# Kernel tuning notes

Hardware: AMD Instinct MI355X
Metric: run time of the kernel (lower is better)

Reference implementation:

```python
import jax, jax.numpy as jnp
import numpy as np

B, C, H, W = 2, 128, 64, 256
G, P, EXP = 8, 4, 2
D = C // G


def _conv1x1(x, w, b):
    # x: (b,c,h,w), w: (o,c), b: (o,)
    return jnp.einsum('bchw,oc->bohw', x, w) + b[None, :, None, None]


def _lin_sample(value, x):
    # value: (b,g,d,h,w); x: (b,g,p,h,w) pixel coords along W -> (b,g,d,p,h,w)
    Bv, Gv, Dv, Hv, Wv = value.shape
    Pv = x.shape[2]
    xc = jnp.clip(x, 0.0, Wv - 1.0)
    x0 = jnp.floor(xc)
    i0 = x0.astype(jnp.int32)
    i1 = jnp.minimum(i0 + 1, Wv - 1)
    t = (xc - x0)[:, :, None]  # (b,g,1,p,h,w)
    shape = (Bv, Gv, Dv, Pv, Hv, Wv)
    v = jnp.broadcast_to(value[:, :, :, None], shape)
    v0 = jnp.take_along_axis(v, jnp.broadcast_to(i0[:, :, None], shape), axis=-1)
    v1 = jnp.take_along_axis(v, jnp.broadcast_to(i1[:, :, None], shape), axis=-1)
    return v0 * (1.0 - t) + v1 * t


def _layernorm_c(x, g, b):
    mu = jnp.mean(x, axis=1, keepdims=True)
    var = jnp.mean((x - mu) ** 2, axis=1, keepdims=True)
    return (x - mu) * jax.lax.rsqrt(var + 1e-5) * g[None, :, None, None] + b[None, :, None, None]


def _forward(ml, mr, fl, fr, nl, nr, gml, gmr, cap, gap,
             wv, bv, wn, bn, woc, boc, wog, bog, wa, ba, wo, bo,
             lw, lb, w1, b1, w2, b2):
    mask = jnp.concatenate([gml, gmr], axis=0)   # (2B,1,H,W)
    q = jnp.concatenate([ml, mr], axis=0)        # (2B,C,H,W)
    ctx = jnp.concatenate([fr, fl], axis=0)      # cross: right feats for left queries
    geo = jnp.concatenate([nr, nl], axis=0)      # (2B,3,H,W)
    B2 = q.shape[0]
    # deformable 1D cross-attention (normal-guided)
    value = _conv1x1(ctx, wv, bv).reshape(B2, G, D, H, W)
    nfeat = _conv1x1(geo, wn, bn).reshape(B2, G, D, H, W)
    off_c = _conv1x1(q, woc, boc).reshape(B2, G, P, H, W)
    off_g = _conv1x1(q, wog, bog).reshape(B2, G, P, H, W)
    attn = jax.nn.softmax(_conv1x1(q, wa, ba).reshape(B2, G, 2 * P, H, W), axis=2)
    ctx_kp = jnp.clip(cap * (W - 1.0) + off_c, 0.0, W - 1.0)
    geo_kp = jnp.clip(gap * (W - 1.0) + off_g, 0.0, W - 1.0)
    s_ctx = _lin_sample(value, ctx_kp)           # (2B,G,D,P,H,W)
    s_geo = _lin_sample(nfeat, geo_kp)
    sampled = jnp.concatenate([s_ctx, s_geo], axis=3)  # (2B,G,D,2P,H,W)
    agg = jnp.einsum('bgdphw,bgphw->bgdhw', sampled, attn).reshape(B2, C, H, W)
    upd = _conv1x1(agg, wo, bo) * mask
    # residual + LayerNorm over channels + 1x1-conv FFN
    x = q + upd
    x = _layernorm_c(x, lw, lb)
    h1 = _conv1x1(x, w1, b1)
    x = x + _conv1x1(h1 * jax.nn.sigmoid(h1), w2, b2)
    return x, ctx_kp, geo_kp


def setup_inputs() -> dict:
    key = jax.random.key(0)
    ks = jax.random.split(key, 20)
    f32 = jnp.float32
    def n(k, shape, s=1.0):
        return jax.random.normal(k, shape, dtype=f32) * s
    return {
        'match_left': n(ks[0], (B, C, H, W)),
        'match_right': n(ks[1], (B, C, H, W)),
        'feat_left': n(ks[2], (B, C, H, W)),
        'feat_right': n(ks[3], (B, C, H, W)),
        'normal_left': n(ks[4], (B, 3, H, W)),
        'normal_right': n(ks[5], (B, 3, H, W)),
        'gate_mask_left': jax.random.uniform(ks[6], (B, 1, H, W), dtype=f32),
        'gate_mask_right': jax.random.uniform(ks[7], (B, 1, H, W), dtype=f32),
        'context_anchor_points': jax.random.uniform(ks[8], (2 * B, G, P, H, W), dtype=f32),
        'geometric_anchor_points': jax.random.uniform(ks[9], (2 * B, G, P, H, W), dtype=f32),
        'w_value': n(ks[10], (C, C), 0.02), 'b_value': jnp.zeros((C,), f32),
        'w_normal': n(ks[11], (C, 3), 0.02), 'b_normal': jnp.zeros((C,), f32),
        'w_off_ctx': n(ks[12], (G * P, C), 0.02), 'b_off_ctx': jnp.zeros((G * P,), f32),
        'w_off_geo': n(ks[13], (G * P, C), 0.02), 'b_off_geo': jnp.zeros((G * P,), f32),
        'w_attn': n(ks[14], (G * 2 * P, C), 0.02), 'b_attn': jnp.zeros((G * 2 * P,), f32),
        'w_out': n(ks[15], (C, C), 0.02), 'b_out': jnp.zeros((C,), f32),
        'ln_w': jnp.ones((C,), f32), 'ln_b': jnp.zeros((C,), f32),
        'w_ff1': n(ks[16], (EXP * C, C), 0.02), 'b_ff1': jnp.zeros((EXP * C,), f32),
        'w_ff2': n(ks[17], (C, EXP * C), 0.02), 'b_ff2': jnp.zeros((C,), f32),
    }


def reference(match_left, match_right, feat_left, feat_right, normal_left, normal_right,
              gate_mask_left, gate_mask_right, context_anchor_points, geometric_anchor_points,
              w_value, b_value, w_normal, b_normal, w_off_ctx, b_off_ctx, w_off_geo, b_off_geo,
              w_attn, b_attn, w_out, b_out, ln_w, ln_b, w_ff1, b_ff1, w_ff2, b_ff2):
    x, ckp, gkp = _forward(match_left, match_right, feat_left, feat_right, normal_left, normal_right,
                           gate_mask_left, gate_mask_right, context_anchor_points, geometric_anchor_points,
                           w_value, b_value, w_normal, b_normal, w_off_ctx, b_off_ctx, w_off_geo, b_off_geo,
                           w_attn, b_attn, w_out, b_out, ln_w, ln_b, w_ff1, b_ff1, w_ff2, b_ff2)
    ml, mr = jnp.split(x, 2, axis=0)
    return (ml, mr, ckp, gkp)
```

## Files before the change

### kernel.cpp

```cpp
#include <hip/hip_runtime.h>
#include <cstdint>
#include <math.h>

#define B2v 4
#define Cc  128
#define Hh  64
#define Ww  256
#define Gg  8
#define Pp  4
#define HW  (Hh*Ww)
#define CHW (Cc*HW)
#define PIT 136

typedef float f32x4 __attribute__((ext_vector_type(4)));
typedef short s16x8 __attribute__((ext_vector_type(8)));
typedef short s16x4 __attribute__((ext_vector_type(4)));

__device__ __forceinline__ short f2bf(float x) {
    union { float f; unsigned u; } a; a.f = x;
    unsigned r = a.u + 0x7fffu + ((a.u >> 16) & 1u);
    return (short)(r >> 16);
}
__device__ __forceinline__ float bf2f(short s) {
    union { unsigned u; float f; } a; a.u = ((unsigned)(unsigned short)s) << 16;
    return a.f;
}
__device__ __forceinline__ unsigned pack2_bf(float f0, float f1) {
    union { float f; unsigned u; } a, b; a.f = f0; b.f = f1;
    return __builtin_amdgcn_perm(b.u, a.u, 0x07060302);
}

__global__ __launch_bounds__(256) void prep_kernel(
    const float* __restrict__ wv, const float* __restrict__ woc,
    const float* __restrict__ wog, const float* __restrict__ wa,
    const float* __restrict__ wo, const float* __restrict__ w1,
    const float* __restrict__ w2,
    const float* __restrict__ boc, const float* __restrict__ bog,
    const float* __restrict__ ba,
    short* __restrict__ wbf, float* __restrict__ bq)
{
    int i = blockIdx.x * 256 + threadIdx.x;
    if (i < 16384) wbf[i] = f2bf(wv[i]);
    else if (i < 32768) {
        int j = i - 16384; int r = j >> 7, c = j & 127;
        float v = (r < 32) ? woc[r * 128 + c] : (r < 64) ? wog[(r - 32) * 128 + c]
                                              : wa[(r - 64) * 128 + c];
        wbf[i] = f2bf(v);
    }
    else if (i < 49152)  wbf[i] = f2bf(wo[i - 32768]);
    else if (i < 81920)  wbf[i] = f2bf(w1[i - 49152]);
    else if (i < 114688) wbf[i] = f2bf(w2[i - 81920]);
    else if (i < 114816) {
        int r = i - 114688;
        bq[r] = (r < 32) ? boc[r] : (r < 64) ? bog[r - 32] : ba[r - 64];
    }
}

__global__ __launch_bounds__(512, 2) void mega_kernel(
    const float* __restrict__ mlq, const float* __restrict__ mrq,
    const float* __restrict__ fl,  const float* __restrict__ fr,
    const float* __restrict__ nl,  const float* __restrict__ nr,
    const float* __restrict__ gml, const float* __restrict__ gmr,
    const float* __restrict__ cap, const float* __restrict__ gap,
    const short* __restrict__ wbf, const float* __restrict__ bq,
    const float* __restrict__ bv,
    const float* __restrict__ wn,  const float* __restrict__ bn,
    const float* __restrict__ bo,
    const float* __restrict__ lnw, const float* __restrict__ lnb,
    const float* __restrict__ b1,  const float* __restrict__ b2,
    float* __restrict__ out_ml, float* __restrict__ out_mr,
    float* __restrict__ ckp_out, float* __restrict__ gkp_out)
{
    __shared__ short buf1[256 * PIT];
    __shared__ short buf2[256 * PIT];
    __shared__ float sgeo[3 * 256];
    __shared__ float swn4[128 * 4];
    __shared__ float redS[512], redQ[512];
    __shared__ float smu[256], srs[256];

    const short* wv_bf = wbf;
    const short* wq_bf = wbf + 16384;
    const short* wo_bf = wbf + 32768;
    const short* w1_bf = wbf + 49152;
    const short* w2_bf = wbf + 81920;

    const int t    = threadIdx.x;
    const int lane = t & 63;
    const int ww   = t >> 6;
    const int lm   = lane & 15;
    const int lq   = lane >> 4;
    const int h = blockIdx.x, b = blockIdx.y;
    const int hWw = h * Ww;
    const int px   = t & 255;
    const int half = t >> 8;

    const float* ctx = (b < 2) ? fr + (size_t)b * CHW : fl + (size_t)(b - 2) * CHW;
    const float* q   = (b < 2) ? mlq + (size_t)b * CHW : mrq + (size_t)(b - 2) * CHW;
    const float* geo = (b < 2) ? nr + (size_t)b * 3 * HW : nl + (size_t)(b - 2) * 3 * HW;
    const float* msk = (b < 2) ? gml + (size_t)b * HW : gmr + (size_t)(b - 2) * HW;
    float* outp = (b < 2) ? out_ml + (size_t)b * CHW : out_mr + (size_t)(b - 2) * CHW;

    for (int i = t; i < 768; i += 512) sgeo[i] = geo[(size_t)(i >> 8) * HW + hWw + (i & 255)];
    if (t < 128) {
        swn4[t * 4 + 0] = wn[t * 3 + 0];
        swn4[t * 4 + 1] = wn[t * 3 + 1];
        swn4[t * 4 + 2] = wn[t * 3 + 2];
        swn4[t * 4 + 3] = bn[t];
    }

    {
        const int c0 = ww * 16;
#pragma unroll
        for (int sub = 0; sub < 4; sub++) {
            const int p = sub * 64 + lane;
            const size_t base = (size_t)c0 * HW + hWw + p;
#pragma unroll
            for (int k = 0; k < 8; k++) {
                float f0 = ctx[base + (size_t)(2 * k) * HW];
                float f1 = ctx[base + (size_t)(2 * k + 1) * HW];
                *(unsigned*)(&buf1[p * PIT + c0 + 2 * k]) = pack2_bf(f0, f1);
            }
        }
    }
    __syncthreads();

    {
        f32x4 acc[16];
#pragma unroll
        for (int nt = 0; nt < 16; nt++) acc[nt] = (f32x4){0.f, 0.f, 0.f, 0.f};
#pragma unroll
        for (int kk = 0; kk < 4; kk++) {
            s16x8 a = *(const s16x8*)(wv_bf + (size_t)(ww * 16 + lm) * 128 + kk * 32 + lq * 8);
#pragma unroll
            for (int nt = 0; nt < 16; nt++) {
                s16x8 bfv = *(const s16x8*)(&buf1[(nt * 16 + lm) * PIT + kk * 32 + lq * 8]);
                acc[nt] = __builtin_amdgcn_mfma_f32_16x16x32_bf16(a, bfv, acc[nt], 0, 0, 0);
            }
        }
        const int ob = ww * 16 + lq * 4;
        float bias[4];
#pragma unroll
        for (int r = 0; r < 4; r++) bias[r] = bv[ob + r];
#pragma unroll
        for (int nt = 0; nt < 16; nt++) {
            const int wg = nt * 16 + lm;
            s16x4 pk;
#pragma unroll
            for (int r = 0; r < 4; r++) pk[r] = f2bf(acc[nt][r] + bias[r]);
            *(s16x4*)(&buf2[wg * PIT + ob]) = pk;
        }
    }
    __syncthreads();

    {
        const int c0 = ww * 16;
#pragma unroll
        for (int sub = 0; sub < 4; sub++) {
            const int p = sub * 64 + lane;
            const size_t base = (size_t)c0 * HW + hWw + p;
#pragma unroll
            for (int k = 0; k < 8; k++) {
                float f0 = q[base + (size_t)(2 * k) * HW];
                float f1 = q[base + (size_t)(2 * k + 1) * HW];
                *(unsigned*)(&buf1[p * PIT + c0 + 2 * k]) = pack2_bf(f0, f1);
            }
        }
    }
    __syncthreads();

    {
        f32x4 acc[16];
#pragma unroll
        for (int nt = 0; nt < 16; nt++) acc[nt] = (f32x4){0.f, 0.f, 0.f, 0.f};
#pragma unroll
        for (int kk = 0; kk < 4; kk++) {
            s16x8 a = *(const s16x8*)(wq_bf + (size_t)(ww * 16 + lm) * 128 + kk * 32 + lq * 8);
#pragma unroll
            for (int nt = 0; nt < 16; nt++) {
                s16x8 bfv = *(const s16x8*)(&buf1[(nt * 16 + lm) * PIT + kk * 32 + lq * 8]);
                acc[nt] = __builtin_amdgcn_mfma_f32_16x16x32_bf16(a, bfv, acc[nt], 0, 0, 0);
            }
        }
        __syncthreads();
        const int ob = ww * 16 + lq * 4;
        float bias[4];
#pragma unroll
        for (int r = 0; r < 4; r++) bias[r] = bq[ob + r];
#pragma unroll
        for (int nt = 0; nt < 16; nt++) {
            const int wg = nt * 16 + lm;
            s16x4 pk;
#pragma unroll
            for (int r = 0; r < 4; r++) pk[r] = f2bf(acc[nt][r] + bias[r]);
            *(s16x4*)(&buf1[wg * PIT + ob]) = pk;
        }
    }
    __syncthreads();

    float attnr[4][8], kpr[4][8];
#pragma unroll
    for (int gi = 0; gi < 4; gi++) {
        const int g = half * 4 + gi;
        s16x8 lg = *(const s16x8*)(&buf1[px * PIT + 64 + g * 8]);
        float L[8], m = -1e30f;
#pragma unroll
        for (int j = 0; j < 8; j++) { L[j] = bf2f(lg[j]); m = fmaxf(m, L[j]); }
        float s = 0.f;
#pragma unroll
        for (int j = 0; j < 8; j++) { L[j] = expf(L[j] - m); s += L[j]; }
        float inv = 1.f / s;
#pragma unroll
        for (int j = 0; j < 8; j++) attnr[gi][j] = L[j] * inv;
#pragma unroll
        for (int p = 0; p < 4; p++) {
            size_t kidx = ((((size_t)b * Gg + g) * Pp + p) * Hh + h) * Ww + px;
            float oc = bf2f(buf1[px * PIT + g * 4 + p]);
            float og = bf2f(buf1[px * PIT + 32 + g * 4 + p]);
            float ck = fminf(fmaxf(cap[kidx] * 255.0f + oc, 0.f), 255.f);
            float gk = fminf(fmaxf(gap[kidx] * 255.0f + og, 0.f), 255.f);
            ckp_out[kidx] = ck;
            gkp_out[kidx] = gk;
            kpr[gi][p] = ck;
            kpr[gi][4 + p] = gk;
        }
    }
    __syncthreads();

#pragma unroll
    for (int gi = 0; gi < 4; gi++) {
        const int g = half * 4 + gi;
        float a16[16];
#pragma unroll
        for (int d = 0; d < 16; d++) a16[d] = 0.f;
#pragma unroll
        for (int j = 0; j < 4; j++) {
            float x = kpr[gi][j];
            int i0 = (int)floorf(x);
            int i1 = min(i0 + 1, Ww - 1);
            float tt = x - (float)i0;
            float c0 = attnr[gi][j] * (1.f - tt);
            float c1 = attnr[gi][j] * tt;
            s16x8 v0a = *(const s16x8*)(&buf2[i0 * PIT + g * 16]);
            s16x8 v0b = *(const s16x8*)(&buf2[i0 * PIT + g * 16 + 8]);
            s16x8 v1a = *(const s16x8*)(&buf2[i1 * PIT + g * 16]);
            s16x8 v1b = *(const s16x8*)(&buf2[i1 * PIT + g * 16 + 8]);
#pragma unroll
            for (int d = 0; d < 8; d++) {
                a16[d]     += c0 * bf2f(v0a[d]) + c1 * bf2f(v1a[d]);
                a16[8 + d] += c0 * bf2f(v0b[d]) + c1 * bf2f(v1b[d]);
            }
        }
        {
            float gs0 = 0.f, gs1 = 0.f, gs2 = 0.f, as = 0.f;
#pragma unroll
            for (int j = 4; j < 8; j++) {
                float x = kpr[gi][j];
                int i0 = (int)floorf(x);
                int i1 = min(i0 + 1, Ww - 1);
                float tt = x - (float)i0;
                float c0 = attnr[gi][j] * (1.f - tt);
                float c1 = attnr[gi][j] * tt;
                gs0 += c0 * sgeo[i0] + c1 * sgeo[i1];
                gs1 += c0 * sgeo[256 + i0] + c1 * sgeo[256 + i1];
                gs2 += c0 * sgeo[512 + i0] + c1 * sgeo[512 + i1];
                as  += attnr[gi][j];
            }
#pragma unroll
            for (int d = 0; d < 16; d++) {
                const float* w4 = &swn4[(g * 16 + d) * 4];
                a16[d] += w4[0] * gs0 + w4[1] * gs1 + w4[2] * gs2 + w4[3] * as;
            }
        }
        s16x8 p0, p1;
#pragma unroll
        for (int d = 0; d < 8; d++) { p0[d] = f2bf(a16[d]); p1[d] = f2bf(a16[8 + d]); }
        *(s16x8*)(&buf1[px * PIT + g * 16])     = p0;
        *(s16x8*)(&buf1[px * PIT + g * 16 + 8]) = p1;
    }
    __syncthreads();

    {
        f32x4 acc1[16];
#pragma unroll
        for (int nt = 0; nt < 16; nt++) acc1[nt] = (f32x4){0.f, 0.f, 0.f, 0.f};
#pragma unroll
        for (int kk = 0; kk < 4; kk++) {
            s16x8 a = *(const s16x8*)(wo_bf + (size_t)(ww * 16 + lm) * 128 + kk * 32 + lq * 8);
#pragma unroll
            for (int nt = 0; nt < 16; nt++) {
                s16x8 bfv = *(const s16x8*)(&buf1[(nt * 16 + lm) * PIT + kk * 32 + lq * 8]);
                acc1[nt] = __builtin_amdgcn_mfma_f32_16x16x32_bf16(a, bfv, acc1[nt], 0, 0, 0);
            }
        }
        __syncthreads();
        const int ob = ww * 16 + lq * 4;
        float bias[4];
#pragma unroll
        for (int r = 0; r < 4; r++) bias[r] = bo[ob + r];
#pragma unroll
        for (int nt = 0; nt < 16; nt++) {
            const int wg = nt * 16 + lm;
            float mval = msk[hWw + wg];
            s16x4 pk;
#pragma unroll
            for (int r = 0; r < 4; r++) {
                float upd = acc1[nt][r] + bias[r];
                float qv = q[(size_t)(ob + r) * HW + hWw + wg];
                pk[r] = f2bf(qv + upd * mval);
            }
            *(s16x4*)(&buf1[wg * PIT + ob]) = pk;
        }
    }
    __syncthreads();

    {
        float ls = 0.f, lsq = 0.f;
#pragma unroll
        for (int c8 = 0; c8 < 8; c8++) {
            s16x8 v = *(const s16x8*)(&buf1[px * PIT + half * 64 + c8 * 8]);
#pragma unroll
            for (int j = 0; j < 8; j++) { float f = bf2f(v[j]); ls += f; lsq += f * f; }
        }
        redS[t] = ls; redQ[t] = lsq;
        __syncthreads();
        if (t < 256) {
            float s  = redS[t] + redS[t + 256];
            float qq = redQ[t] + redQ[t + 256];
            float mu = s * (1.f / 128.f);
            float var = qq * (1.f / 128.f) - mu * mu;
            smu[t] = mu;
            srs[t] = rsqrtf(var + 1e-5f);
        }
        __syncthreads();
        const float mu = smu[px], rs = srs[px];
#pragma unroll
        for (int c8 = 0; c8 < 8; c8++) {
            s16x8 v = *(const s16x8*)(&buf1[px * PIT + half * 64 + c8 * 8]);
            s16x8 pk;
#pragma unroll
            for (int j = 0; j < 8; j++) {
                int c = half * 64 + c8 * 8 + j;
                pk[j] = f2bf((bf2f(v[j]) - mu) * rs * lnw[c] + lnb[c]);
            }
            *(s16x8*)(&buf1[px * PIT + half * 64 + c8 * 8]) = pk;
        }
    }
    __syncthreads();

    f32x4 acc3[16];
#pragma unroll
    for (int nt = 0; nt < 16; nt++) acc3[nt] = (f32x4){0.f, 0.f, 0.f, 0.f};

    for (int jc = 0; jc < 2; jc++) {
        f32x4 acc2[16];
#pragma unroll
        for (int nt = 0; nt < 16; nt++) acc2[nt] = (f32x4){0.f, 0.f, 0.f, 0.f};
#pragma unroll
        for (int kk = 0; kk < 4; kk++) {
            s16x8 a = *(const s16x8*)(w1_bf + (size_t)(jc * 128 + ww * 16 + lm) * 128 + kk * 32 + lq * 8);
#pragma unroll
            for (int nt = 0; nt < 16; nt++) {
                s16x8 bfv = *(const s16x8*)(&buf1[(nt * 16 + lm) * PIT + kk * 32 + lq * 8]);
                acc2[nt] = __builtin_amdgcn_mfma_f32_16x16x32_bf16(a, bfv, acc2[nt], 0, 0, 0);
            }
        }
        {
            const int jb = ww * 16 + lq * 4;
            float bias[4];
#pragma unroll
            for (int r = 0; r < 4; r++) bias[r] = b1[jc * 128 + jb + r];
#pragma unroll
            for (int nt = 0; nt < 16; nt++) {
                const int wg = nt * 16 + lm;
                s16x4 pk;
#pragma unroll
                for (int r = 0; r < 4; r++) {
                    float hv = acc2[nt][r] + bias[r];
                    pk[r] = f2bf(hv / (1.f + expf(-hv)));
                }
                *(s16x4*)(&buf2[wg * PIT + jb]) = pk;
            }
        }
        __syncthreads();
#pragma unroll
        for (int kk = 0; kk < 4; kk++) {
            s16x8 a = *(const s16x8*)(w2_bf + (size_t)(ww * 16 + lm) * 256 + jc * 128 + kk * 32 + lq * 8);
#pragma unroll
            for (int nt = 0; nt < 16; nt++) {
                s16x8 bfv = *(const s16x8*)(&buf2[(nt * 16 + lm) * PIT + kk * 32 + lq * 8]);
                acc3[nt] = __builtin_amdgcn_mfma_f32_16x16x32_bf16(a, bfv, acc3[nt], 0, 0, 0);
            }
        }
        __syncthreads();
    }

    {
        const int ob = ww * 16 + lq * 4;
        float b2v[4];
#pragma unroll
        for (int r = 0; r < 4; r++) b2v[r] = b2[ob + r];
#pragma unroll
        for (int nt = 0; nt < 16; nt++) {
            const int wg = nt * 16 + lm;
            s16x4 xn4 = *(const s16x4*)(&buf1[wg * PIT + ob]);
#pragma unroll
            for (int r = 0; r < 4; r++)
                outp[(size_t)(ob + r) * HW + hWw + wg] = bf2f(xn4[r]) + b2v[r] + acc3[nt][r];
        }
    }
}

extern "C" void kernel_launch(void* const* d_in, const int* in_sizes, int n_in,
                              void* d_out, int out_size, void* d_ws, size_t ws_size,
                              hipStream_t stream)
{
    const float* match_l = (const float*)d_in[0];
    const float* match_r = (const float*)d_in[1];
    const float* feat_l  = (const float*)d_in[2];
    const float* feat_r  = (const float*)d_in[3];
    const float* norm_l  = (const float*)d_in[4];
    const float* norm_r  = (const float*)d_in[5];
    const float* gml     = (const float*)d_in[6];
    const float* gmr     = (const float*)d_in[7];
    const float* cap     = (const float*)d_in[8];
    const float* gap     = (const float*)d_in[9];
    const float* wv  = (const float*)d_in[10]; const float* bv  = (const float*)d_in[11];
    const float* wn  = (const float*)d_in[12]; const float* bn  = (const float*)d_in[13];
    const float* woc = (const float*)d_in[14]; const float* boc = (const float*)d_in[15];
    const float* wog = (const float*)d_in[16]; const float* bog = (const float*)d_in[17];
    const float* wa  = (const float*)d_in[18]; const float* ba  = (const float*)d_in[19];
    const float* wo  = (const float*)d_in[20]; const float* bo  = (const float*)d_in[21];
    const float* lnw = (const float*)d_in[22]; const float* lnb = (const float*)d_in[23];
    const float* w1  = (const float*)d_in[24]; const float* b1  = (const float*)d_in[25];
    const float* w2  = (const float*)d_in[26]; const float* b2  = (const float*)d_in[27];

    float* out = (float*)d_out;
    float* out_ml  = out;
    float* out_mr  = out + (size_t)2 * CHW;
    float* ckp_out = out + (size_t)4 * CHW;
    float* gkp_out = ckp_out + (size_t)B2v * Gg * Pp * HW;

    float* ws = (float*)d_ws;
    float* bq  = ws;
    short* wbf = (short*)(bq + 128);

    prep_kernel<<<dim3(449), dim3(256), 0, stream>>>(
        wv, woc, wog, wa, wo, w1, w2, boc, bog, ba, wbf, bq);
    mega_kernel<<<dim3(Hh, B2v), dim3(512), 0, stream>>>(
        match_l, match_r, feat_l, feat_r, norm_l, norm_r, gml, gmr, cap, gap,
        wbf, bq, bv, wn, bn, bo, lnw, lnb, b1, b2,
        out_ml, out_mr, ckp_out, gkp_out);
}
```

Baseline: 223.6 us.

## Vectorize input staging, merge GEMM phases, use hardware bf16 pack and fast math

Loads ctx and q with float4 global reads into two separate LDS buffers in a single phase, which drops two barriers and lets the value and query projections run back to back. It prefetches anchor points into registers, packs LDS constants (geo as float4, normal weights as pairs, LN params), and converts to bf16 with the v_cvt_pk_bf16_f32 instruction. It also swaps expf, division and rsqrt for the fast hardware intrinsics, and uses packed float2 math in the sampling loop. The costs are higher register pressure from the prefetched arrays and slightly lower precision in softmax, SiLU and LayerNorm.

```diff
diff --git a/kernel.cpp b/kernel.cpp
--- a/kernel.cpp
+++ b/kernel.cpp
@@ -13,6 +13,7 @@
 #define PIT 136
 
 typedef float f32x4 __attribute__((ext_vector_type(4)));
+typedef float f32x2 __attribute__((ext_vector_type(2)));
 typedef short s16x8 __attribute__((ext_vector_type(8)));
 typedef short s16x4 __attribute__((ext_vector_type(4)));
 
@@ -25,10 +26,18 @@
     union { unsigned u; float f; } a; a.u = ((unsigned)(unsigned short)s) << 16;
     return a.f;
 }
-__device__ __forceinline__ unsigned pack2_bf(float f0, float f1) {
-    union { float f; unsigned u; } a, b; a.f = f0; b.f = f1;
-    return __builtin_amdgcn_perm(b.u, a.u, 0x07060302);
-}
+__device__ __forceinline__ unsigned cvtpk(float lo, float hi) {
+    unsigned r;
+    asm("v_cvt_pk_bf16_f32 %0, %1, %2" : "=v"(r) : "v"(lo), "v"(hi));
+    return r;
+}
+__device__ __forceinline__ f32x2 unpk(unsigned w) {
+    union { unsigned u; float f; } lo, hi;
+    lo.u = w << 16; hi.u = w & 0xffff0000u;
+    return (f32x2){lo.f, hi.f};
+}
+__device__ __forceinline__ float frcp(float x) { return __builtin_amdgcn_rcpf(x); }
+__device__ __forceinline__ float fexp(float x) { return __expf(x); }
 
 __global__ __launch_bounds__(256) void prep_kernel(
     const float* __restrict__ wv, const float* __restrict__ woc,
@@ -73,8 +82,9 @@
 {
     __shared__ short buf1[256 * PIT];
     __shared__ short buf2[256 * PIT];
-    __shared__ float sgeo[3 * 256];
-    __shared__ float swn4[128 * 4];
+    __shared__ f32x4 sgeo4[256];
+    __shared__ f32x2 swnp[256];
+    __shared__ float sln[256];
     __shared__ float redS[512], redQ[512];
     __shared__ float smu[256], srs[256];
 
@@ -100,43 +110,81 @@
     const float* msk = (b < 2) ? gml + (size_t)b * HW : gmr + (size_t)(b - 2) * HW;
     float* outp = (b < 2) ? out_ml + (size_t)b * CHW : out_mr + (size_t)(b - 2) * CHW;
 
-    for (int i = t; i < 768; i += 512) sgeo[i] = geo[(size_t)(i >> 8) * HW + hWw + (i & 255)];
-    if (t < 128) {
-        swn4[t * 4 + 0] = wn[t * 3 + 0];
-        swn4[t * 4 + 1] = wn[t * 3 + 1];
-        swn4[t * 4 + 2] = wn[t * 3 + 2];
-        swn4[t * 4 + 3] = bn[t];
+    float capr[16], gapr[16];
+    const size_t kbase = ((size_t)b * Gg + half * 4) * Pp * (size_t)HW + hWw + px;
+    {
+#pragma unroll
+        for (int i = 0; i < 16; i++) {
+            capr[i] = cap[kbase + (size_t)i * HW];
+            gapr[i] = gap[kbase + (size_t)i * HW];
+        }
+    }
+
+    if (t < 256) {
+        sgeo4[t] = (f32x4){geo[hWw + t], geo[HW + hWw + t], geo[2 * HW + hWw + t], 0.f};
+        const int pr = t >> 2, m = t & 3;
+        const int ch0 = pr * 2, ch1 = ch0 + 1;
+        float a0 = (m < 3) ? wn[ch0 * 3 + m] : bn[ch0];
+        float a1 = (m < 3) ? wn[ch1 * 3 + m] : bn[ch1];
+        swnp[t] = (f32x2){a0, a1};
+    }
+    else {
+        int i = t - 256;
+        sln[i] = (i < 128) ? lnw[i] : lnb[i - 128];
     }
 
     {
         const int c0 = ww * 16;
-#pragma unroll
-        for (int sub = 0; sub < 4; sub++) {
-            const int p = sub * 64 + lane;
-            const size_t base = (size_t)c0 * HW + hWw + p;
-#pragma unroll
-            for (int k = 0; k < 8; k++) {
-                float f0 = ctx[base + (size_t)(2 * k) * HW];
-                float f1 = ctx[base + (size_t)(2 * k + 1) * HW];
-                *(unsigned*)(&buf1[p * PIT + c0 + 2 * k]) = pack2_bf(f0, f1);
-            }
-        }
-    }
-    __syncthreads();
-
-    {
-        f32x4 acc[16];
-#pragma unroll
-        for (int nt = 0; nt < 16; nt++) acc[nt] = (f32x4){0.f, 0.f, 0.f, 0.f};
-#pragma unroll
-        for (int kk = 0; kk < 4; kk++) {
-            s16x8 a = *(const s16x8*)(wv_bf + (size_t)(ww * 16 + lm) * 128 + kk * 32 + lq * 8);
-#pragma unroll
-            for (int nt = 0; nt < 16; nt++) {
-                s16x8 bfv = *(const s16x8*)(&buf1[(nt * 16 + lm) * PIT + kk * 32 + lq * 8]);
-                acc[nt] = __builtin_amdgcn_mfma_f32_16x16x32_bf16(a, bfv, acc[nt], 0, 0, 0);
-            }
-        }
+        const int p0 = lane * 4;
+        const size_t gbase = (size_t)c0 * HW + hWw + p0;
+        {
+            f32x4 L[16];
+#pragma unroll
+            for (int c = 0; c < 16; c++) L[c] = *(const f32x4*)(ctx + gbase + (size_t)c * HW);
+#pragma unroll
+            for (int j = 0; j < 4; j++) {
+                uint4 w0, w1;
+                w0.x = cvtpk(L[0][j],  L[1][j]);  w0.y = cvtpk(L[2][j],  L[3][j]);
+                w0.z = cvtpk(L[4][j],  L[5][j]);  w0.w = cvtpk(L[6][j],  L[7][j]);
+                w1.x = cvtpk(L[8][j],  L[9][j]);  w1.y = cvtpk(L[10][j], L[11][j]);
+                w1.z = cvtpk(L[12][j], L[13][j]); w1.w = cvtpk(L[14][j], L[15][j]);
+                *(uint4*)(&buf1[(p0 + j) * PIT + c0])     = w0;
+                *(uint4*)(&buf1[(p0 + j) * PIT + c0 + 8]) = w1;
+            }
+        }
+        {
+            f32x4 L[16];
+#pragma unroll
+            for (int c = 0; c < 16; c++) L[c] = *(const f32x4*)(q + gbase + (size_t)c * HW);
+#pragma unroll
+            for (int j = 0; j < 4; j++) {
+                uint4 w0, w1;
+                w0.x = cvtpk(L[0][j],  L[1][j]);  w0.y = cvtpk(L[2][j],  L[3][j]);
+                w0.z = cvtpk(L[4][j],  L[5][j]);  w0.w = cvtpk(L[6][j],  L[7][j]);
+                w1.x = cvtpk(L[8][j],  L[9][j]);  w1.y = cvtpk(L[10][j], L[11][j]);
+                w1.z = cvtpk(L[12][j], L[13][j]); w1.w = cvtpk(L[14][j], L[15][j]);
+                *(uint4*)(&buf2[(p0 + j) * PIT + c0])     = w0;
+                *(uint4*)(&buf2[(p0 + j) * PIT + c0 + 8]) = w1;
+            }
+        }
+    }
+    __syncthreads();
+
+    f32x4 accv[16];
+#pragma unroll
+    for (int nt = 0; nt < 16; nt++) accv[nt] = (f32x4){0.f, 0.f, 0.f, 0.f};
+#pragma unroll
+    for (int kk = 0; kk < 4; kk++) {
+        s16x8 a = *(const s16x8*)(wv_bf + (size_t)(ww * 16 + lm) * 128 + kk * 32 + lq * 8);
+#pragma unroll
+        for (int nt = 0; nt < 16; nt++) {
+            s16x8 bfv = *(const s16x8*)(&buf1[(nt * 16 + lm) * PIT + kk * 32 + lq * 8]);
+            accv[nt] = __builtin_amdgcn_mfma_f32_16x16x32_bf16(a, bfv, accv[nt], 0, 0, 0);
+        }
+    }
+    __syncthreads();
+
+    {
         const int ob = ww * 16 + lq * 4;
         float bias[4];
 #pragma unroll
@@ -144,44 +192,27 @@
 #pragma unroll
         for (int nt = 0; nt < 16; nt++) {
             const int wg = nt * 16 + lm;
-            s16x4 pk;
-#pragma unroll
-            for (int r = 0; r < 4; r++) pk[r] = f2bf(acc[nt][r] + bias[r]);
-            *(s16x4*)(&buf2[wg * PIT + ob]) = pk;
-        }
-    }
-    __syncthreads();
-
-    {
-        const int c0 = ww * 16;
-#pragma unroll
-        for (int sub = 0; sub < 4; sub++) {
-            const int p = sub * 64 + lane;
-            const size_t base = (size_t)c0 * HW + hWw + p;
-#pragma unroll
-            for (int k = 0; k < 8; k++) {
-                float f0 = q[base + (size_t)(2 * k) * HW];
-                float f1 = q[base + (size_t)(2 * k + 1) * HW];
-                *(unsigned*)(&buf1[p * PIT + c0 + 2 * k]) = pack2_bf(f0, f1);
-            }
-        }
-    }
-    __syncthreads();
-
-    {
-        f32x4 acc[16];
-#pragma unroll
-        for (int nt = 0; nt < 16; nt++) acc[nt] = (f32x4){0.f, 0.f, 0.f, 0.f};
-#pragma unroll
-        for (int kk = 0; kk < 4; kk++) {
-            s16x8 a = *(const s16x8*)(wq_bf + (size_t)(ww * 16 + lm) * 128 + kk * 32 + lq * 8);
-#pragma unroll
-            for (int nt = 0; nt < 16; nt++) {
-                s16x8 bfv = *(const s16x8*)(&buf1[(nt * 16 + lm) * PIT + kk * 32 + lq * 8]);
-                acc[nt] = __builtin_amdgcn_mfma_f32_16x16x32_bf16(a, bfv, acc[nt], 0, 0, 0);
-            }
-        }
-        __syncthreads();
+            uint2 pk;
+            pk.x = cvtpk(accv[nt][0] + bias[0], accv[nt][1] + bias[1]);
+            pk.y = cvtpk(accv[nt][2] + bias[2], accv[nt][3] + bias[3]);
+            *(uint2*)(&buf1[wg * PIT + ob]) = pk;
+        }
+    }
+    f32x4 accp[16];
+#pragma unroll
+    for (int nt = 0; nt < 16; nt++) accp[nt] = (f32x4){0.f, 0.f, 0.f, 0.f};
+#pragma unroll
+    for (int kk = 0; kk < 4; kk++) {
+        s16x8 a = *(const s16x8*)(wq_bf + (size_t)(ww * 16 + lm) * 128 + kk * 32 + lq * 8);
+#pragma unroll
+        for (int nt = 0; nt < 16; nt++) {
+            s16x8 bfv = *(const s16x8*)(&buf2[(nt * 16 + lm) * PIT + kk * 32 + lq * 8]);
+            accp[nt] = __builtin_amdgcn_mfma_f32_16x16x32_bf16(a, bfv, accp[nt], 0, 0, 0);
+        }
+    }
+    __syncthreads();
+
+    {
         const int ob = ww * 16 + lq * 4;
         float bias[4];
 #pragma unroll
@@ -189,10 +220,10 @@
 #pragma unroll
         for (int nt = 0; nt < 16; nt++) {
             const int wg = nt * 16 + lm;
-            s16x4 pk;
-#pragma unroll
-            for (int r = 0; r < 4; r++) pk[r] = f2bf(acc[nt][r] + bias[r]);
-            *(s16x4*)(&buf1[wg * PIT + ob]) = pk;
+            uint2 pk;
+            pk.x = cvtpk(accp[nt][0] + bias[0], accp[nt][1] + bias[1]);
+            pk.y = cvtpk(accp[nt][2] + bias[2], accp[nt][3] + bias[3]);
+            *(uint2*)(&buf2[wg * PIT + ob]) = pk;
         }
     }
     __syncthreads();
@@ -201,23 +232,23 @@
 #pragma unroll
     for (int gi = 0; gi < 4; gi++) {
         const int g = half * 4 + gi;
-        s16x8 lg = *(const s16x8*)(&buf1[px * PIT + 64 + g * 8]);
+        s16x8 lg = *(const s16x8*)(&buf2[px * PIT + 64 + g * 8]);
         float L[8], m = -1e30f;
 #pragma unroll
         for (int j = 0; j < 8; j++) { L[j] = bf2f(lg[j]); m = fmaxf(m, L[j]); }
         float s = 0.f;
 #pragma unroll
-        for (int j = 0; j < 8; j++) { L[j] = expf(L[j] - m); s += L[j]; }
-        float inv = 1.f / s;
+        for (int j = 0; j < 8; j++) { L[j] = fexp(L[j] - m); s += L[j]; }
+        float inv = frcp(s);
 #pragma unroll
         for (int j = 0; j < 8; j++) attnr[gi][j] = L[j] * inv;
 #pragma unroll
         for (int p = 0; p < 4; p++) {
-            size_t kidx = ((((size_t)b * Gg + g) * Pp + p) * Hh + h) * Ww + px;
-            float oc = bf2f(buf1[px * PIT + g * 4 + p]);
-            float og = bf2f(buf1[px * PIT + 32 + g * 4 + p]);
-            float ck = fminf(fmaxf(cap[kidx] * 255.0f + oc, 0.f), 255.f);
-            float gk = fminf(fmaxf(gap[kidx] * 255.0f + og, 0.f), 255.f);
+            size_t kidx = kbase + (size_t)(gi * 4 + p) * HW;
+            float oc = bf2f(buf2[px * PIT + g * 4 + p]);
+            float og = bf2f(buf2[px * PIT + 32 + g * 4 + p]);
+            float ck = fminf(fmaxf(capr[gi * 4 + p] * 255.0f + oc, 0.f), 255.f);
+            float gk = fminf(fmaxf(gapr[gi * 4 + p] * 255.0f + og, 0.f), 255.f);
             ckp_out[kidx] = ck;
             gkp_out[kidx] = gk;
             kpr[gi][p] = ck;
@@ -229,53 +260,60 @@
 #pragma unroll
     for (int gi = 0; gi < 4; gi++) {
         const int g = half * 4 + gi;
-        float a16[16];
-#pragma unroll
-        for (int d = 0; d < 16; d++) a16[d] = 0.f;
+        f32x2 A[8];
+#pragma unroll
+        for (int k = 0; k < 8; k++) A[k] = (f32x2){0.f, 0.f};
 #pragma unroll
         for (int j = 0; j < 4; j++) {
             float x = kpr[gi][j];
-            int i0 = (int)floorf(x);
+            float fx = floorf(x);
+            int i0 = (int)fx;
             int i1 = min(i0 + 1, Ww - 1);
-            float tt = x - (float)i0;
+            float tt = x - fx;
             float c0 = attnr[gi][j] * (1.f - tt);
             float c1 = attnr[gi][j] * tt;
-            s16x8 v0a = *(const s16x8*)(&buf2[i0 * PIT + g * 16]);
-            s16x8 v0b = *(const s16x8*)(&buf2[i0 * PIT + g * 16 + 8]);
-            s16x8 v1a = *(const s16x8*)(&buf2[i1 * PIT + g * 16]);
-            s16x8 v1b = *(const s16x8*)(&buf2[i1 * PIT + g * 16 + 8]);
-#pragma unroll
-            for (int d = 0; d < 8; d++) {
-                a16[d]     += c0 * bf2f(v0a[d]) + c1 * bf2f(v1a[d]);
-                a16[8 + d] += c0 * bf2f(v0b[d]) + c1 * bf2f(v1b[d]);
-            }
+            f32x2 c0v = {c0, c0}, c1v = {c1, c1};
+            uint4 v0a = *(const uint4*)(&buf1[i0 * PIT + g * 16]);
+            uint4 v0b = *(const uint4*)(&buf1[i0 * PIT + g * 16 + 8]);
+            uint4 v1a = *(const uint4*)(&buf1[i1 * PIT + g * 16]);
+            uint4 v1b = *(const uint4*)(&buf1[i1 * PIT + g * 16 + 8]);
+            const unsigned w0[8] = {v0a.x, v0a.y, v0a.z, v0a.w, v0b.x, v0b.y, v0b.z, v0b.w};
+            const unsigned w1[8] = {v1a.x, v1a.y, v1a.z, v1a.w, v1b.x, v1b.y, v1b.z, v1b.w};
+#pragma unroll
+            for (int k = 0; k < 8; k++)
+                A[k] += unpk(w0[k]) * c0v + unpk(w1[k]) * c1v;
         }
         {
             float gs0 = 0.f, gs1 = 0.f, gs2 = 0.f, as = 0.f;
 #pragma unroll
             for (int j = 4; j < 8; j++) {
                 float x = kpr[gi][j];
-                int i0 = (int)floorf(x);
+                float fx = floorf(x);
+                int i0 = (int)fx;
                 int i1 = min(i0 + 1, Ww - 1);
-                float tt = x - (float)i0;
+                float tt = x - fx;
                 float c0 = attnr[gi][j] * (1.f - tt);
                 float c1 = attnr[gi][j] * tt;
-                gs0 += c0 * sgeo[i0] + c1 * sgeo[i1];
-                gs1 += c0 * sgeo[256 + i0] + c1 * sgeo[256 + i1];
-                gs2 += c0 * sgeo[512 + i0] + c1 * sgeo[512 + i1];
+                f32x4 ga = sgeo4[i0], gb = sgeo4[i1];
+                gs0 += c0 * ga[0] + c1 * gb[0];
+                gs1 += c0 * ga[1] + c1 * gb[1];
+                gs2 += c0 * ga[2] + c1 * gb[2];
                 as  += attnr[gi][j];
             }
-#pragma unroll
-            for (int d = 0; d < 16; d++) {
-                const float* w4 = &swn4[(g * 16 + d) * 4];
-                a16[d] += w4[0] * gs0 + w4[1] * gs1 + w4[2] * gs2 + w4[3] * as;
-            }
-        }
-        s16x8 p0, p1;
-#pragma unroll
-        for (int d = 0; d < 8; d++) { p0[d] = f2bf(a16[d]); p1[d] = f2bf(a16[8 + d]); }
-        *(s16x8*)(&buf1[px * PIT + g * 16])     = p0;
-        *(s16x8*)(&buf1[px * PIT + g * 16 + 8]) = p1;
+            f32x2 g0v = {gs0, gs0}, g1v = {gs1, gs1}, g2v = {gs2, gs2}, asv = {as, as};
+#pragma unroll
+            for (int k = 0; k < 8; k++) {
+                const f32x2* wp = &swnp[(g * 8 + k) * 4];
+                A[k] += wp[0] * g0v + wp[1] * g1v + wp[2] * g2v + wp[3] * asv;
+            }
+        }
+        uint4 o0, o1;
+        o0.x = cvtpk(A[0][0], A[0][1]); o0.y = cvtpk(A[1][0], A[1][1]);
+        o0.z = cvtpk(A[2][0], A[2][1]); o0.w = cvtpk(A[3][0], A[3][1]);
+        o1.x = cvtpk(A[4][0], A[4][1]); o1.y = cvtpk(A[5][0], A[5][1]);
+        o1.z = cvtpk(A[6][0], A[6][1]); o1.w = cvtpk(A[7][0], A[7][1]);
+        *(uint4*)(&buf2[px * PIT + g * 16])     = o0;
+        *(uint4*)(&buf2[px * PIT + g * 16 + 8]) = o1;
     }
     __syncthreads();
 
@@ -288,11 +326,10 @@
             s16x8 a = *(const s16x8*)(wo_bf + (size_t)(ww * 16 + lm) * 128 + kk * 32 + lq * 8);
 #pragma unroll
             for (int nt = 0; nt < 16; nt++) {
-                s16x8 bfv = *(const s16x8*)(&buf1[(nt * 16 + lm) * PIT + kk * 32 + lq * 8]);
+                s16x8 bfv = *(const s16x8*)(&buf2[(nt * 16 + lm) * PIT + kk * 32 + lq * 8]);
                 acc1[nt] = __builtin_amdgcn_mfma_f32_16x16x32_bf16(a, bfv, acc1[nt], 0, 0, 0);
             }
         }
-        __syncthreads();
         const int ob = ww * 16 + lq * 4;
         float bias[4];
 #pragma unroll
@@ -301,14 +338,17 @@
         for (int nt = 0; nt < 16; nt++) {
             const int wg = nt * 16 + lm;
             float mval = msk[hWw + wg];
-            s16x4 pk;
+            float xv[4];
 #pragma unroll
             for (int r = 0; r < 4; r++) {
                 float upd = acc1[nt][r] + bias[r];
                 float qv = q[(size_t)(ob + r) * HW + hWw + wg];
-                pk[r] = f2bf(qv + upd * mval);
-            }
-            *(s16x4*)(&buf1[wg * PIT + ob]) = pk;
+                xv[r] = qv + upd * mval;
+            }
+            uint2 pk;
+            pk.x = cvtpk(xv[0], xv[1]);
+            pk.y = cvtpk(xv[2], xv[3]);
+            *(uint2*)(&buf1[wg * PIT + ob]) = pk;
         }
     }
     __syncthreads();
@@ -317,9 +357,14 @@
         float ls = 0.f, lsq = 0.f;
 #pragma unroll
         for (int c8 = 0; c8 < 8; c8++) {
-            s16x8 v = *(const s16x8*)(&buf1[px * PIT + half * 64 + c8 * 8]);
-#pragma unroll
-            for (int j = 0; j < 8; j++) { float f = bf2f(v[j]); ls += f; lsq += f * f; }
+            uint4 u = *(const uint4*)(&buf1[px * PIT + half * 64 + c8 * 8]);
+            const unsigned wv4[4] = {u.x, u.y, u.z, u.w};
+#pragma unroll
+            for (int j2 = 0; j2 < 4; j2++) {
+                f32x2 e = unpk(wv4[j2]);
+                ls  += e[0] + e[1];
+                lsq += e[0] * e[0] + e[1] * e[1];
+            }
         }
         redS[t] = ls; redQ[t] = lsq;
         __syncthreads();
@@ -329,20 +374,27 @@
             float mu = s * (1.f / 128.f);
             float var = qq * (1.f / 128.f) - mu * mu;
             smu[t] = mu;
-            srs[t] = rsqrtf(var + 1e-5f);
+            srs[t] = __builtin_amdgcn_rsqf(var + 1e-5f);
         }
         __syncthreads();
         const float mu = smu[px], rs = srs[px];
 #pragma unroll
         for (int c8 = 0; c8 < 8; c8++) {
-            s16x8 v = *(const s16x8*)(&buf1[px * PIT + half * 64 + c8 * 8]);
-            s16x8 pk;
-#pragma unroll
-            for (int j = 0; j < 8; j++) {
-                int c = half * 64 + c8 * 8 + j;
-                pk[j] = f2bf((bf2f(v[j]) - mu) * rs * lnw[c] + lnb[c]);
-            }
-            *(s16x8*)(&buf1[px * PIT + half * 64 + c8 * 8]) = pk;
+            const int cb = half * 64 + c8 * 8;
+            uint4 u = *(const uint4*)(&buf1[px * PIT + cb]);
+            const unsigned wv4[4] = {u.x, u.y, u.z, u.w};
+            uint4 o;
+            unsigned res[4];
+#pragma unroll
+            for (int j2 = 0; j2 < 4; j2++) {
+                f32x2 e = unpk(wv4[j2]);
+                const int c = cb + j2 * 2;
+                float a0 = rs * sln[c],     bb0 = sln[128 + c]     - mu * a0;
+                float a1 = rs * sln[c + 1], bb1 = sln[128 + c + 1] - mu * a1;
+                res[j2] = cvtpk(e[0] * a0 + bb0, e[1] * a1 + bb1);
+            }
+            o.x = res[0]; o.y = res[1]; o.z = res[2]; o.w = res[3];
+            *(uint4*)(&buf1[px * PIT + cb]) = o;
         }
     }
     __syncthreads();
@@ -372,13 +424,16 @@
 #pragma unroll
             for (int nt = 0; nt < 16; nt++) {
                 const int wg = nt * 16 + lm;
-                s16x4 pk;
+                float o[4];
 #pragma unroll
                 for (int r = 0; r < 4; r++) {
                     float hv = acc2[nt][r] + bias[r];
-                    pk[r] = f2bf(hv / (1.f + expf(-hv)));
+                    o[r] = hv * frcp(1.f + fexp(-hv));
                 }
-                *(s16x4*)(&buf2[wg * PIT + jb]) = pk;
+                uint2 pk;
+                pk.x = cvtpk(o[0], o[1]);
+                pk.y = cvtpk(o[2], o[3]);
+                *(uint2*)(&buf2[wg * PIT + jb]) = pk;
             }
         }
         __syncthreads();
```

After: 206.8 us. -7.5%, faster.
